# Performance work log

Measured on AMD Instinct MI355X. Metric: run time of the kernel, lower is better.

## Reference

```python
import jax, jax.numpy as jnp
import numpy as np

GROUPS = 32  # min(32, 256//4)
EPS = 1e-5


def setup_inputs() -> dict:
    key = jax.random.key(0)
    ks = jax.random.split(key, 4)
    B, C, H, W = 8, 256, 128, 128
    x = jax.random.normal(ks[0], (B, C, H, W), dtype=jnp.float32)
    gn_w = jnp.ones((C,), dtype=jnp.float32)
    gn_b = jnp.zeros((C,), dtype=jnp.float32)
    qkv_w = jax.random.normal(ks[1], (3 * C, C), dtype=jnp.float32) * (C ** -0.5)
    qkv_b = jnp.zeros((3 * C,), dtype=jnp.float32)
    proj_w = jax.random.normal(ks[2], (C, C), dtype=jnp.float32) * (C ** -0.5)
    proj_b = jnp.zeros((C,), dtype=jnp.float32)
    return {"x": x, "gn_w": gn_w, "gn_b": gn_b, "qkv_w": qkv_w,
            "qkv_b": qkv_b, "proj_w": proj_w, "proj_b": proj_b}


def _group_norm(x, w, b):
    B, C, H, W = x.shape
    xg = x.reshape(B, GROUPS, C // GROUPS, H, W)
    mean = xg.mean(axis=(2, 3, 4), keepdims=True)
    var = xg.var(axis=(2, 3, 4), keepdims=True)
    xg = (xg - mean) * jax.lax.rsqrt(var + EPS)
    x = xg.reshape(B, C, H, W)
    return x * w[None, :, None, None] + b[None, :, None, None]


def reference(x, gn_w, gn_b, qkv_w, qkv_b, proj_w, proj_b):
    B, C, H, W = x.shape
    num_heads = 8
    head_dim = C // num_heads
    scale = head_dim ** -0.5

    h = _group_norm(x, gn_w, gn_b)
    # 1x1 conv == per-pixel matmul over channels
    qkv = jnp.einsum('bchw,oc->bohw', h, qkv_w) + qkv_b[None, :, None, None]
    qkv = qkv.reshape(B, 3, num_heads, head_dim, H * W)
    q, k, v = qkv[:, 0], qkv[:, 1], qkv[:, 2]  # each (B, h, head_dim, HW)
    # Faithful to source: contracts over spatial axis d=HW -> (B,h,hd,hd)
    attn = jnp.einsum('bhid,bhjd->bhij', q, k) * scale
    attn = jax.nn.softmax(attn, axis=-1)
    out = jnp.einsum('bhij,bhjd->bhid', attn, v)  # (B, h, head_dim, HW)
    out = out.reshape(B, C, H, W)
    out = jnp.einsum('bchw,oc->bohw', out, proj_w) + proj_b[None, :, None, None]
    return x + out
```

## Files before the change

kernel.cpp:

```cpp
#include <hip/hip_runtime.h>
#include <stdint.h>

typedef __bf16 bf16;
typedef __attribute__((ext_vector_type(8))) __bf16 bf16x8;
typedef __attribute__((ext_vector_type(4))) float f32x4;

#define S_HW 16384
#define N_C 256

__device__ __forceinline__ f32x4 mfma16(bf16x8 a, bf16x8 b, f32x4 c) {
  return __builtin_amdgcn_mfma_f32_16x16x32_bf16(a, b, c, 0, 0, 0);
}
__device__ __forceinline__ void async_ld16(const bf16* g, bf16* l) {
  __builtin_amdgcn_global_load_lds(
      (const __attribute__((address_space(1))) unsigned int*)g,
      (__attribute__((address_space(3))) unsigned int*)l, 16, 0, 0);
}
__device__ __forceinline__ unsigned short bf2u(bf16 h) {
  union { bf16 h; unsigned short u; } c; c.h = h; return c.u;
}
__device__ __forceinline__ bf16 u2bf(unsigned short u) {
  union { unsigned short u; bf16 h; } c; c.u = u; return c.h;
}

__global__ __launch_bounds__(256) void k_split(
    const float* __restrict__ x, bf16* __restrict__ yhi, bf16* __restrict__ ylo,
    bf16* __restrict__ yt, float* __restrict__ Sx) {
  int b = blockIdx.z, c0 = blockIdx.y * 64, s0 = blockIdx.x * 64;
  __shared__ unsigned T[64][65];
  __shared__ float sxl[256];
  int t = threadIdx.x;
  int cl = t >> 2, sg = t & 3;
  size_t off = (size_t)(b * N_C + c0 + cl) * S_HW + s0 + sg * 16;
  const float* xp = x + off;
  bf16x8 hv[2], lv[2];
  float sum = 0.f;
#pragma unroll
  for (int i2 = 0; i2 < 4; i2++) {
    float4 v = *(const float4*)(xp + i2 * 4);
    float f4[4] = {v.x, v.y, v.z, v.w};
#pragma unroll
    for (int k = 0; k < 4; k++) {
      int i = i2 * 4 + k;
      float fv = f4[k];
      bf16 h = (bf16)fv;
      bf16 l = (bf16)(fv - (float)h);
      hv[i >> 3][i & 7] = h;
      lv[i >> 3][i & 7] = l;
      sum += fv;
      T[sg * 16 + i][cl] = (unsigned)bf2u(h) | ((unsigned)bf2u(l) << 16);
    }
  }
  *(bf16x8*)(yhi + off) = hv[0];
  *(bf16x8*)(yhi + off + 8) = hv[1];
  *(bf16x8*)(ylo + off) = lv[0];
  *(bf16x8*)(ylo + off + 8) = lv[1];
  sxl[t] = sum;
  __syncthreads();
  if (t < 64) {
    float s2 = sxl[t * 4] + sxl[t * 4 + 1] + sxl[t * 4 + 2] + sxl[t * 4 + 3];
    atomicAdd(&Sx[b * N_C + c0 + t], s2);
  }
  int sl = t >> 2, cg = t & 3;
  bf16x8 ho[2], lo2[2];
#pragma unroll
  for (int i = 0; i < 16; i++) {
    unsigned u = T[sl][cg * 16 + i];
    ho[i >> 3][i & 7] = u2bf((unsigned short)(u & 0xffffu));
    lo2[i >> 3][i & 7] = u2bf((unsigned short)(u >> 16));
  }
  size_t tb = (size_t)(b * S_HW + s0 + sl) * 512 + c0 + cg * 16;
  *(bf16x8*)(yt + tb) = ho[0];
  *(bf16x8*)(yt + tb + 8) = ho[1];
  *(bf16x8*)(yt + tb + 256) = lo2[0];
  *(bf16x8*)(yt + tb + 256 + 8) = lo2[1];
}

__global__ __launch_bounds__(256) void k_gram(
    const bf16* __restrict__ yhi, const bf16* __restrict__ ylo,
    float* __restrict__ YG3) {
  constexpr int BK = 32;
  constexpr int NT = 64;
  constexpr int BUF = 128 * BK;
  __shared__ __align__(16) bf16 As[3 * BUF];
  __shared__ __align__(16) bf16 Bs[3 * BUF];
  int kc = blockIdx.x * 2048;
  int m0 = (blockIdx.y >> 2) * 128, n0 = (blockIdx.y & 3) * 128;
  int b = blockIdx.z;
  int tid = threadIdx.x, lane = tid & 63, wave = tid >> 6;
  int wm = (wave >> 1) * 64, wn = (wave & 1) * 64;
  const bf16* Ab = yhi + (size_t)(b * N_C + m0) * S_HW;
  const bf16* Bb = (n0 < 256) ? yhi + (size_t)(b * N_C + n0) * S_HW
                              : ylo + (size_t)(b * N_C + n0 - 256) * S_HW;
  f32x4 acc[4][4] = {};
  int fm = lane & 15, fk = (lane >> 4) * 8;

  auto STAGE = [&](int bi, int t) {
    int kt = kc + t * BK;
#pragma unroll
    for (int i = 0; i < 2; i++) {
      int ch = i * 256 + tid;
      int row = ch >> 2, col = (ch & 3) * 8;
      async_ld16(Ab + (size_t)row * S_HW + kt + col,
                 As + bi * BUF + (i * 256 + wave * 64) * 8);
      async_ld16(Bb + (size_t)row * S_HW + kt + col,
                 Bs + bi * BUF + (i * 256 + wave * 64) * 8);
    }
  };

  STAGE(0, 0);
  STAGE(1, 1);
  STAGE(2, 2);
  int bi = 0;
  for (int t = 0; t < NT - 2; t++) {
    asm volatile("s_waitcnt vmcnt(8)" ::: "memory");
    __builtin_amdgcn_s_barrier();
    const bf16* Ap = As + bi * BUF;
    const bf16* Bp = Bs + bi * BUF;
    bf16x8 af[4], bfr[4];
#pragma unroll
    for (int q = 0; q < 4; q++) {
      af[q] = *(const bf16x8*)(Ap + (wm + q * 16 + fm) * BK + fk);
      bfr[q] = *(const bf16x8*)(Bp + (wn + q * 16 + fm) * BK + fk);
    }
    asm volatile("s_waitcnt lgkmcnt(0)" ::: "memory");
    __builtin_amdgcn_sched_barrier(0);
    __builtin_amdgcn_s_barrier();
    if (t + 3 < NT) STAGE(bi, t + 3);
#pragma unroll
    for (int ti = 0; ti < 4; ti++)
#pragma unroll
      for (int tj = 0; tj < 4; tj++)
        acc[ti][tj] = mfma16(af[ti], bfr[tj], acc[ti][tj]);
    bi = (bi == 2) ? 0 : bi + 1;
  }
#pragma unroll
  for (int pe = 0; pe < 2; pe++) {
    if (pe == 0)
      asm volatile("s_waitcnt vmcnt(4)" ::: "memory");
    else
      asm volatile("s_waitcnt vmcnt(0)" ::: "memory");
    __builtin_amdgcn_s_barrier();
    const bf16* Ap = As + bi * BUF;
    const bf16* Bp = Bs + bi * BUF;
    bf16x8 af[4], bfr[4];
#pragma unroll
    for (int q = 0; q < 4; q++) {
      af[q] = *(const bf16x8*)(Ap + (wm + q * 16 + fm) * BK + fk);
      bfr[q] = *(const bf16x8*)(Bp + (wn + q * 16 + fm) * BK + fk);
    }
#pragma unroll
    for (int ti = 0; ti < 4; ti++)
#pragma unroll
      for (int tj = 0; tj < 4; tj++)
        acc[ti][tj] = mfma16(af[ti], bfr[tj], acc[ti][tj]);
    bi = (bi == 2) ? 0 : bi + 1;
  }
  int quad = lane >> 4, cn = lane & 15;
#pragma unroll
  for (int ti = 0; ti < 4; ti++)
#pragma unroll
    for (int r = 0; r < 4; r++) {
      int m = m0 + wm + ti * 16 + quad * 4 + r;
#pragma unroll
      for (int tj = 0; tj < 4; tj++) {
        int n = n0 + wn + tj * 16 + cn;
        atomicAdd(&YG3[(size_t)(b * N_C + m) * 512 + n], acc[ti][tj][r]);
      }
    }
}

__global__ __launch_bounds__(256) void k_wkt(const float* __restrict__ qkv_w,
                                             float* __restrict__ WkT) {
  int k = blockIdx.x, j = threadIdx.x;
  WkT[k * 256 + j] = qkv_w[(256 + j) * 256 + k];
}

__global__ __launch_bounds__(256) void k_coefs(
    const float* __restrict__ Sx, const float* __restrict__ YG3,
    const float* __restrict__ gn_w, const float* __restrict__ gn_b,
    const float* __restrict__ qkv_w, const float* __restrict__ qkv_b,
    float* __restrict__ a_, float* __restrict__ bv_, float* __restrict__ u_,
    float* __restrict__ vbe) {
  int b = blockIdx.x, role = blockIdx.y, t = threadIdx.x;
  __shared__ float sxl[256], gxd[256], gm[32], gr[32], sh[256], bl[256];
  __shared__ float ured[64][4];
  sxl[t] = Sx[b * N_C + t];
  gxd[t] = YG3[(size_t)(b * N_C + t) * 512 + t] +
           2.f * YG3[(size_t)(b * N_C + t) * 512 + 256 + t];
  __syncthreads();
  if (t < 32) {
    float s = 0.f, q2 = 0.f;
#pragma unroll
    for (int i = 0; i < 8; i++) { s += sxl[t * 8 + i]; q2 += gxd[t * 8 + i]; }
    float mean = s * (1.f / 131072.f);
    float var = q2 * (1.f / 131072.f) - mean * mean;
    gm[t] = mean;
    gr[t] = 1.f / sqrtf(var + 1e-5f);
  }
  __syncthreads();
  {
    float A = gn_w[t] * gr[t >> 3];
    float B = gn_b[t] - gm[t >> 3] * A;
    bl[t] = B;
    sh[t] = A * sxl[t] + 16384.f * B;
    if (role == 0) {
      a_[b * N_C + t] = A;
      bv_[b * N_C + t] = B;
    }
  }
  __syncthreads();
  if (role == 0) {
    const float* wp = qkv_w + (size_t)(512 + t) * 256;
    float acc = 0.f;
    for (int c = 0; c < 256; c++) acc += wp[c] * bl[c];
    vbe[b * N_C + t] = acc + qkv_b[512 + t];
  } else {
    int r = (role - 1) * 64 + (t >> 2);
    int seg = (t & 3) * 64;
    const float* wp = qkv_w + (size_t)r * 256 + seg;
    float p = 0.f;
    for (int c = 0; c < 64; c++) p += wp[c] * sh[seg + c];
    ured[t >> 2][t & 3] = p;
    __syncthreads();
    if (t < 64)
      u_[b * 512 + (role - 1) * 64 + t] =
          ured[t][0] + ured[t][1] + ured[t][2] + ured[t][3];
  }
}

__global__ __launch_bounds__(256) void k_t1(
    const float* __restrict__ YG3, const float* __restrict__ WkT,
    const float* __restrict__ a_, const float* __restrict__ bv_,
    const float* __restrict__ Sx, float* __restrict__ T1) {
  int tile = blockIdx.x, b = blockIdx.y;
  int i0 = (tile >> 2) * 64, j0 = (tile & 3) * 64;
  __shared__ float As[64][69];
  __shared__ float Bs[64][69];
  __shared__ float al[256], bl[256], sxl[256];
  int t = threadIdx.x;
  al[t] = a_[b * N_C + t];
  bl[t] = bv_[b * N_C + t];
  sxl[t] = Sx[b * N_C + t];
  int cl = t >> 2, qq = (t & 3) * 16;
  int kk = t >> 2, jj = (t & 3) * 16;
  int ti = t >> 4, tj = t & 15;
  float acc[4][4] = {};
  for (int kc = 0; kc < 256; kc += 64) {
    {
      const float* yg = YG3 + (size_t)(b * N_C + i0 + cl) * 512 + kc + qq;
#pragma unroll
      for (int i = 0; i < 16; i++) As[cl][qq + i] = yg[i] + yg[256 + i];
    }
    __syncthreads();
    {
      int cp = kc + kk;
      const float* ygp = YG3 + (size_t)(b * N_C + cp) * 512 + 256 + i0 + jj;
#pragma unroll
      for (int i = 0; i < 16; i++) As[jj + i][kk] += ygp[i];
    }
    __syncthreads();
    {
      int c = i0 + cl;
      float ac = al[c], bc = bl[c], sxc = sxl[c];
#pragma unroll
      for (int i = 0; i < 16; i++) {
        int cp = kc + qq + i;
        As[cl][qq + i] = ac * al[cp] * As[cl][qq + i] + ac * bl[cp] * sxc +
                         bc * al[cp] * sxl[cp] + 16384.f * bc * bl[cp];
      }
    }
    {
      const float* wp = WkT + (size_t)(kc + kk) * 256 + j0 + jj;
#pragma unroll
      for (int i = 0; i < 16; i += 4) {
        float4 v = *(const float4*)(wp + i);
        Bs[kk][jj + i] = v.x; Bs[kk][jj + i + 1] = v.y;
        Bs[kk][jj + i + 2] = v.z; Bs[kk][jj + i + 3] = v.w;
      }
    }
    __syncthreads();
    for (int k = 0; k < 64; k++) {
      float av[4], bv4[4];
#pragma unroll
      for (int ii = 0; ii < 4; ii++) av[ii] = As[ti * 4 + ii][k];
#pragma unroll
      for (int j2 = 0; j2 < 4; j2++) bv4[j2] = Bs[k][tj * 4 + j2];
#pragma unroll
      for (int ii = 0; ii < 4; ii++)
#pragma unroll
        for (int j2 = 0; j2 < 4; j2++) acc[ii][j2] += av[ii] * bv4[j2];
    }
    __syncthreads();
  }
#pragma unroll
  for (int ii = 0; ii < 4; ii++)
#pragma unroll
    for (int j2 = 0; j2 < 4; j2++)
      T1[(size_t)(b * N_C + i0 + ti * 4 + ii) * 256 + j0 + tj * 4 + j2] =
          acc[ii][j2];
}

__global__ __launch_bounds__(256) void k_logits(
    const float* __restrict__ T1, const float* __restrict__ qkv_w,
    const float* __restrict__ qkv_b, const float* __restrict__ u_,
    float* __restrict__ attn) {
  int h = blockIdx.x, b = blockIdx.y;
  __shared__ float Tc[64][33];
  __shared__ float Wql[32][65];
  __shared__ float Ll[32][33];
  __shared__ float uq[32], uk[32], bq[32], bk[32];
  int t = threadIdx.x;
  if (t < 32) {
    uq[t] = u_[b * 512 + h * 32 + t];
    uk[t] = u_[b * 512 + 256 + h * 32 + t];
    bq[t] = qkv_b[h * 32 + t];
    bk[t] = qkv_b[256 + h * 32 + t];
  }
  int i = t & 31, jg = t >> 5;
  float acc[4] = {};
  for (int cc = 0; cc < 256; cc += 64) {
    {
      int c_l = t >> 2, seg = (t & 3) * 8;
      const float* tp = T1 + (size_t)(b * N_C + cc + c_l) * 256 + h * 32 + seg;
      float4 v0 = *(const float4*)tp, v1 = *(const float4*)(tp + 4);
      Tc[c_l][seg] = v0.x; Tc[c_l][seg + 1] = v0.y;
      Tc[c_l][seg + 2] = v0.z; Tc[c_l][seg + 3] = v0.w;
      Tc[c_l][seg + 4] = v1.x; Tc[c_l][seg + 5] = v1.y;
      Tc[c_l][seg + 6] = v1.z; Tc[c_l][seg + 7] = v1.w;
      int row = t >> 3, seg2 = (t & 7) * 8;
      const float* wp = qkv_w + (size_t)(h * 32 + row) * 256 + cc + seg2;
      float4 w0 = *(const float4*)wp, w1 = *(const float4*)(wp + 4);
      Wql[row][seg2] = w0.x; Wql[row][seg2 + 1] = w0.y;
      Wql[row][seg2 + 2] = w0.z; Wql[row][seg2 + 3] = w0.w;
      Wql[row][seg2 + 4] = w1.x; Wql[row][seg2 + 5] = w1.y;
      Wql[row][seg2 + 6] = w1.z; Wql[row][seg2 + 7] = w1.w;
    }
    __syncthreads();
    for (int c = 0; c < 64; c++) {
      float w = Wql[i][c];
#pragma unroll
      for (int j2 = 0; j2 < 4; j2++) acc[j2] += w * Tc[c][jg * 4 + j2];
    }
    __syncthreads();
  }
  const float scale = 0.17677669529663687f;
#pragma unroll
  for (int j2 = 0; j2 < 4; j2++) {
    int j = jg * 4 + j2;
    Ll[i][j] = scale * (acc[j2] + bq[i] * uk[j] + bk[j] * uq[i] +
                        16384.f * bq[i] * bk[j]);
  }
  __syncthreads();
  if (t < 32) {
    float m = -1e30f;
    for (int j = 0; j < 32; j++) m = fmaxf(m, Ll[t][j]);
    float e[32], s = 0.f;
    for (int j = 0; j < 32; j++) { e[j] = expf(Ll[t][j] - m); s += e[j]; }
    float inv = 1.f / s;
    float* ap = attn + (size_t)((b * 8 + h) * 32 + t) * 32;
    for (int j = 0; j < 32; j++) ap[j] = e[j] * inv;
  }
}

__global__ __launch_bounds__(256) void k_pv(
    const float* __restrict__ proj_w, const float* __restrict__ attn,
    const float* __restrict__ qkv_w, const float* __restrict__ a_,
    const float* __restrict__ vbe, const float* __restrict__ proj_b,
    bf16* __restrict__ FA, float* __restrict__ g_) {
  int tile = blockIdx.x, b = blockIdx.y;
  int i0 = (tile >> 2) * 64, j0 = (tile & 3) * 64;
  __shared__ float As[64][69];
  __shared__ float Bs[64][69];
  __shared__ float At[2][32][33];
  __shared__ float gred[64][4];
  int t = threadIdx.x;
  int cl = t >> 2, qq = (t & 3) * 16;
  int kk = t >> 2, jj = (t & 3) * 16;
  int ti = t >> 4, tj = t & 15;
  float acc[4][4] = {};
  float gacc = 0.f;
  for (int kc = 0; kc < 256; kc += 64) {
    int h0 = kc >> 5;
    __syncthreads();
    {
      const float* ap = attn + (size_t)b * 8192 + h0 * 1024;
#pragma unroll
      for (int i = 0; i < 8; i++) {
        int idx = t * 8 + i;
        At[idx >> 10][(idx >> 5) & 31][idx & 31] = ap[idx];
      }
      const float* wp = qkv_w + (size_t)(512 + kc + kk) * 256 + j0 + jj;
#pragma unroll
      for (int i = 0; i < 16; i += 4) {
        float4 v = *(const float4*)(wp + i);
        Bs[kk][jj + i] = v.x; Bs[kk][jj + i + 1] = v.y;
        Bs[kk][jj + i + 2] = v.z; Bs[kk][jj + i + 3] = v.w;
      }
    }
    __syncthreads();
    {
      int hl = qq >> 5;
      int jbase = qq & 31;
      const float* pp = proj_w + (size_t)(i0 + cl) * 256 + (h0 + hl) * 32;
      float pr[32];
#pragma unroll
      for (int i = 0; i < 32; i += 4) {
        float4 v = *(const float4*)(pp + i);
        pr[i] = v.x; pr[i + 1] = v.y; pr[i + 2] = v.z; pr[i + 3] = v.w;
      }
#pragma unroll
      for (int i = 0; i < 16; i++) {
        int jm = jbase + i;
        float s = 0.f;
#pragma unroll
        for (int ii = 0; ii < 32; ii++) s += pr[ii] * At[hl][ii][jm];
        As[cl][qq + i] = s;
        gacc += s * vbe[b * N_C + kc + qq + i];
      }
    }
    __syncthreads();
    for (int k = 0; k < 64; k++) {
      float av[4], bv4[4];
#pragma unroll
      for (int ii = 0; ii < 4; ii++) av[ii] = As[ti * 4 + ii][k];
#pragma unroll
      for (int j2 = 0; j2 < 4; j2++) bv4[j2] = Bs[k][tj * 4 + j2];
#pragma unroll
      for (int ii = 0; ii < 4; ii++)
#pragma unroll
        for (int j2 = 0; j2 < 4; j2++) acc[ii][j2] += av[ii] * bv4[j2];
    }
  }
  __syncthreads();
  gred[cl][t & 3] = gacc;
  __syncthreads();
  if ((tile & 3) == 0 && t < 64)
    g_[b * N_C + i0 + t] =
        gred[t][0] + gred[t][1] + gred[t][2] + gred[t][3] + proj_b[i0 + t];
  float a4[4];
  {
    float4 v = *(const float4*)(a_ + b * N_C + j0 + tj * 4);
    a4[0] = v.x; a4[1] = v.y; a4[2] = v.z; a4[3] = v.w;
  }
#pragma unroll
  for (int ii = 0; ii < 4; ii++) {
    int row = i0 + ti * 4 + ii;
#pragma unroll
    for (int j2 = 0; j2 < 4; j2++) {
      int col = j0 + tj * 4 + j2;
      float f = acc[ii][j2] * a4[j2] + (row == col ? 1.0f : 0.0f);
      bf16 hi = (bf16)f;
      bf16 lo = (bf16)(f - (float)hi);
      FA[(size_t)(b * N_C + row) * 512 + col] = hi;
      FA[(size_t)(b * N_C + row) * 512 + 256 + col] = lo;
    }
  }
}

__global__ __launch_bounds__(512) void k_final(
    const bf16* __restrict__ FA, const bf16* __restrict__ yt,
    const float* __restrict__ g_, float* __restrict__ out) {
  constexpr int BK = 64;
  constexpr int NT = 12;
  constexpr int BUFA = 256 * BK;
  constexpr int BUFB = 128 * BK;
  __shared__ __align__(16) bf16 As[3 * BUFA];
  __shared__ __align__(16) bf16 Bs[3 * BUFB];
  int b = blockIdx.z, n0 = blockIdx.x * 128;
  int tid = threadIdx.x, lane = tid & 63, wave = tid >> 6;
  int wm = (wave >> 1) * 64, wn = (wave & 1) * 64;
  const bf16* Ab = FA + (size_t)b * N_C * 512;
  const bf16* Bb = yt + (size_t)(b * S_HW + n0) * 512;
  f32x4 acc[4][4] = {};
  int fm = lane & 15, cs = lane >> 4;

  auto STAGE = [&](int bi, int t) {
    int kt = t * BK;
    int ka = (kt < 512) ? kt : kt - 512;
    int kb = (kt < 256) ? kt : kt - 256;
#pragma unroll
    for (int i = 0; i < 4; i++) {
      int ch = i * 512 + tid;
      int row = ch >> 3, slot = ch & 7;
      int gcol = (slot ^ (row & 7)) * 8;
      async_ld16(Ab + (size_t)row * 512 + ka + gcol,
                 As + bi * BUFA + ch * 8);
    }
#pragma unroll
    for (int i = 0; i < 2; i++) {
      int ch = i * 512 + tid;
      int row = ch >> 3, slot = ch & 7;
      int gcol = (slot ^ (row & 7)) * 8;
      async_ld16(Bb + (size_t)row * 512 + kb + gcol,
                 Bs + bi * BUFB + ch * 8);
    }
  };

  STAGE(0, 0);
  STAGE(1, 1);
  STAGE(2, 2);
  int bi = 0;
  for (int t = 0; t < NT - 2; t++) {
    asm volatile("s_waitcnt vmcnt(12)" ::: "memory");
    __builtin_amdgcn_s_barrier();
    const bf16* Ap = As + bi * BUFA;
    const bf16* Bp = Bs + bi * BUFB;
    bf16x8 af[4][2], bfr[4][2];
#pragma unroll
    for (int q = 0; q < 4; q++) {
      int ra = wm + q * 16 + fm;
      int rb = wn + q * 16 + fm;
#pragma unroll
      for (int h = 0; h < 2; h++) {
        af[q][h] = *(const bf16x8*)(Ap + ra * BK +
                                    (((h << 2) | cs) ^ (ra & 7)) * 8);
        bfr[q][h] = *(const bf16x8*)(Bp + rb * BK +
                                     (((h << 2) | cs) ^ (rb & 7)) * 8);
      }
    }
    asm volatile("s_waitcnt lgkmcnt(0)" ::: "memory");
    __builtin_amdgcn_sched_barrier(0);
    __builtin_amdgcn_s_barrier();
    if (t + 3 < NT) STAGE(bi, t + 3);
    __builtin_amdgcn_sched_barrier(0);
#pragma unroll
    for (int ti = 0; ti < 4; ti++)
#pragma unroll
      for (int tj = 0; tj < 4; tj++) {
        acc[ti][tj] = mfma16(af[ti][0], bfr[tj][0], acc[ti][tj]);
        acc[ti][tj] = mfma16(af[ti][1], bfr[tj][1], acc[ti][tj]);
      }
    bi = (bi == 2) ? 0 : bi + 1;
  }
#pragma unroll
  for (int pe = 0; pe < 2; pe++) {
    if (pe == 0)
      asm volatile("s_waitcnt vmcnt(6)" ::: "memory");
    else
      asm volatile("s_waitcnt vmcnt(0)" ::: "memory");
    __builtin_amdgcn_s_barrier();
    const bf16* Ap = As + bi * BUFA;
    const bf16* Bp = Bs + bi * BUFB;
    bf16x8 af[4][2], bfr[4][2];
#pragma unroll
    for (int q = 0; q < 4; q++) {
      int ra = wm + q * 16 + fm;
      int rb = wn + q * 16 + fm;
#pragma unroll
      for (int h = 0; h < 2; h++) {
        af[q][h] = *(const bf16x8*)(Ap + ra * BK +
                                    (((h << 2) | cs) ^ (ra & 7)) * 8);
        bfr[q][h] = *(const bf16x8*)(Bp + rb * BK +
                                     (((h << 2) | cs) ^ (rb & 7)) * 8);
      }
    }
#pragma unroll
    for (int ti = 0; ti < 4; ti++)
#pragma unroll
      for (int tj = 0; tj < 4; tj++) {
        acc[ti][tj] = mfma16(af[ti][0], bfr[tj][0], acc[ti][tj]);
        acc[ti][tj] = mfma16(af[ti][1], bfr[tj][1], acc[ti][tj]);
      }
    bi = (bi == 2) ? 0 : bi + 1;
  }
  int quad = lane >> 4, cn = lane & 15;
#pragma unroll
  for (int ti = 0; ti < 4; ti++)
#pragma unroll
    for (int r = 0; r < 4; r++) {
      int row = wm + ti * 16 + quad * 4 + r;
      float gb = g_[b * N_C + row];
#pragma unroll
      for (int tj = 0; tj < 4; tj++) {
        int col = n0 + wn + tj * 16 + cn;
        size_t idx = (size_t)(b * N_C + row) * S_HW + col;
        out[idx] = acc[ti][tj][r] + gb;
      }
    }
}

extern "C" void kernel_launch(void* const* d_in, const int* in_sizes, int n_in,
                              void* d_out, int out_size, void* d_ws,
                              size_t ws_size, hipStream_t stream) {
  const float* x = (const float*)d_in[0];
  const float* gn_w = (const float*)d_in[1];
  const float* gn_b = (const float*)d_in[2];
  const float* qkv_w = (const float*)d_in[3];
  const float* qkv_b = (const float*)d_in[4];
  const float* proj_w = (const float*)d_in[5];
  const float* proj_b = (const float*)d_in[6];
  float* out = (float*)d_out;

  const size_t MB = 1ull << 20;
  char* ws = (char*)d_ws;
  bf16* ylo = (bf16*)ws;
  bf16* yt = (bf16*)(ws + 64 * MB);
  float* YG3 = (float*)(ws + 192 * MB);
  bf16* FA = (bf16*)(ws + 194 * MB);
  float* WkT = (float*)(ws + 196 * MB);
  float* attn = (float*)(ws + 196 * MB + 256 * 1024);
  float* Sx = (float*)(ws + 196 * MB + 512 * 1024);
  float* a_ = (float*)(ws + 196 * MB + 520 * 1024);
  float* bv_ = (float*)(ws + 196 * MB + 528 * 1024);
  float* u_ = (float*)(ws + 196 * MB + 536 * 1024);
  float* vbe = (float*)(ws + 196 * MB + 552 * 1024);
  float* g_ = (float*)(ws + 196 * MB + 560 * 1024);
  float* T1 = (float*)(ws + 198 * MB);
  bf16* yhi = (bf16*)d_out;

  if (ws_size < 200 * MB) return;

  hipMemsetAsync(YG3, 0, 4 * MB + 520 * 1024, stream);
  k_split<<<dim3(256, 4, 8), 256, 0, stream>>>(x, yhi, ylo, yt, Sx);
  k_gram<<<dim3(8, 8, 8), 256, 0, stream>>>(yhi, ylo, YG3);
  k_wkt<<<256, 256, 0, stream>>>(qkv_w, WkT);
  k_coefs<<<dim3(8, 9), 256, 0, stream>>>(Sx, YG3, gn_w, gn_b, qkv_w, qkv_b,
                                          a_, bv_, u_, vbe);
  k_t1<<<dim3(16, 8), 256, 0, stream>>>(YG3, WkT, a_, bv_, Sx, T1);
  k_logits<<<dim3(8, 8), 256, 0, stream>>>(T1, qkv_w, qkv_b, u_, attn);
  k_pv<<<dim3(16, 8), 256, 0, stream>>>(proj_w, attn, qkv_w, a_, vbe, proj_b,
                                        FA, g_);
  k_final<<<dim3(128, 1, 8), 512, 0, stream>>>(FA, yt, g_, out);
}
```

Measured before the change: 520.9 us.

## Enlarge Gram kernel tile to 256x256 with XOR-swizzled LDS and double buffering

Result: no change. 516.1 us (-0.9%).

```diff
diff --git a/kernel.cpp b/kernel.cpp
--- a/kernel.cpp
+++ b/kernel.cpp
@@ -76,96 +76,89 @@
   *(bf16x8*)(yt + tb + 256 + 8) = lo2[1];
 }
 
-__global__ __launch_bounds__(256) void k_gram(
+__global__ __launch_bounds__(512, 2) void k_gram(
     const bf16* __restrict__ yhi, const bf16* __restrict__ ylo,
     float* __restrict__ YG3) {
-  constexpr int BK = 32;
-  constexpr int NT = 64;
-  constexpr int BUF = 128 * BK;
-  __shared__ __align__(16) bf16 As[3 * BUF];
-  __shared__ __align__(16) bf16 Bs[3 * BUF];
-  int kc = blockIdx.x * 2048;
-  int m0 = (blockIdx.y >> 2) * 128, n0 = (blockIdx.y & 3) * 128;
+  constexpr int BK = 64;
+  constexpr int NT = 16;
+  constexpr int BUF = 256 * BK;
+  __shared__ __align__(16) bf16 As[2 * BUF];
+  __shared__ __align__(16) bf16 Bs[2 * BUF];
+  int kc = blockIdx.x * 1024;
+  int nsel = blockIdx.y;
   int b = blockIdx.z;
   int tid = threadIdx.x, lane = tid & 63, wave = tid >> 6;
-  int wm = (wave >> 1) * 64, wn = (wave & 1) * 64;
-  const bf16* Ab = yhi + (size_t)(b * N_C + m0) * S_HW;
-  const bf16* Bb = (n0 < 256) ? yhi + (size_t)(b * N_C + n0) * S_HW
-                              : ylo + (size_t)(b * N_C + n0 - 256) * S_HW;
-  f32x4 acc[4][4] = {};
-  int fm = lane & 15, fk = (lane >> 4) * 8;
+  int wm = (wave >> 1) * 64, wn = (wave & 1) * 128;
+  const bf16* Ab = yhi + (size_t)(b * N_C) * S_HW;
+  const bf16* Bb = (nsel == 0 ? yhi : ylo) + (size_t)(b * N_C) * S_HW;
+  f32x4 acc[4][8] = {};
+  int fm = lane & 15, cs = lane >> 4;
 
   auto STAGE = [&](int bi, int t) {
     int kt = kc + t * BK;
 #pragma unroll
-    for (int i = 0; i < 2; i++) {
-      int ch = i * 256 + tid;
-      int row = ch >> 2, col = (ch & 3) * 8;
-      async_ld16(Ab + (size_t)row * S_HW + kt + col,
-                 As + bi * BUF + (i * 256 + wave * 64) * 8);
-      async_ld16(Bb + (size_t)row * S_HW + kt + col,
-                 Bs + bi * BUF + (i * 256 + wave * 64) * 8);
+    for (int i = 0; i < 4; i++) {
+      int ch = i * 512 + tid;
+      int row = ch >> 3, slot = ch & 7;
+      int gcol = (slot ^ (row & 7)) * 8;
+      async_ld16(Ab + (size_t)row * S_HW + kt + gcol, As + bi * BUF + ch * 8);
+      async_ld16(Bb + (size_t)row * S_HW + kt + gcol, Bs + bi * BUF + ch * 8);
     }
   };
 
   STAGE(0, 0);
   STAGE(1, 1);
-  STAGE(2, 2);
-  int bi = 0;
-  for (int t = 0; t < NT - 2; t++) {
-    asm volatile("s_waitcnt vmcnt(8)" ::: "memory");
+  int cur = 0;
+  for (int t = 0; t < NT; t++) {
+    if (t < NT - 1)
+      asm volatile("s_waitcnt vmcnt(8)" ::: "memory");
+    else
+      asm volatile("s_waitcnt vmcnt(0)" ::: "memory");
     __builtin_amdgcn_s_barrier();
-    const bf16* Ap = As + bi * BUF;
-    const bf16* Bp = Bs + bi * BUF;
-    bf16x8 af[4], bfr[4];
+    const bf16* Ap = As + cur * BUF;
+    const bf16* Bp = Bs + cur * BUF;
+    bf16x8 af[4][2], bfr[8][2];
 #pragma unroll
     for (int q = 0; q < 4; q++) {
-      af[q] = *(const bf16x8*)(Ap + (wm + q * 16 + fm) * BK + fk);
-      bfr[q] = *(const bf16x8*)(Bp + (wn + q * 16 + fm) * BK + fk);
+      int ra = wm + q * 16 + fm;
+#pragma unroll
+      for (int h = 0; h < 2; h++)
+        af[q][h] =
+            *(const bf16x8*)(Ap + ra * BK + (((h << 2) | cs) ^ (ra & 7)) * 8);
+    }
+#pragma unroll
+    for (int p = 0; p < 8; p++) {
+      int rb = wn + p * 16 + fm;
+#pragma unroll
+      for (int h = 0; h < 2; h++)
+        bfr[p][h] =
+            *(const bf16x8*)(Bp + rb * BK + (((h << 2) | cs) ^ (rb & 7)) * 8);
     }
     asm volatile("s_waitcnt lgkmcnt(0)" ::: "memory");
     __builtin_amdgcn_sched_barrier(0);
     __builtin_amdgcn_s_barrier();
-    if (t + 3 < NT) STAGE(bi, t + 3);
-#pragma unroll
-    for (int ti = 0; ti < 4; ti++)
-#pragma unroll
-      for (int tj = 0; tj < 4; tj++)
-        acc[ti][tj] = mfma16(af[ti], bfr[tj], acc[ti][tj]);
-    bi = (bi == 2) ? 0 : bi + 1;
-  }
-#pragma unroll
-  for (int pe = 0; pe < 2; pe++) {
-    if (pe == 0)
-      asm volatile("s_waitcnt vmcnt(4)" ::: "memory");
-    else
-      asm volatile("s_waitcnt vmcnt(0)" ::: "memory");
-    __builtin_amdgcn_s_barrier();
-    const bf16* Ap = As + bi * BUF;
-    const bf16* Bp = Bs + bi * BUF;
-    bf16x8 af[4], bfr[4];
-#pragma unroll
-    for (int q = 0; q < 4; q++) {
-      af[q] = *(const bf16x8*)(Ap + (wm + q * 16 + fm) * BK + fk);
-      bfr[q] = *(const bf16x8*)(Bp + (wn + q * 16 + fm) * BK + fk);
-    }
-#pragma unroll
-    for (int ti = 0; ti < 4; ti++)
-#pragma unroll
-      for (int tj = 0; tj < 4; tj++)
-        acc[ti][tj] = mfma16(af[ti], bfr[tj], acc[ti][tj]);
-    bi = (bi == 2) ? 0 : bi + 1;
+    if (t + 2 < NT) STAGE(cur, t + 2);
+    __builtin_amdgcn_sched_barrier(0);
+#pragma unroll
+    for (int q = 0; q < 4; q++)
+#pragma unroll
+      for (int p = 0; p < 8; p++) {
+        acc[q][p] = mfma16(af[q][0], bfr[p][0], acc[q][p]);
+        acc[q][p] = mfma16(af[q][1], bfr[p][1], acc[q][p]);
+      }
+    cur ^= 1;
   }
   int quad = lane >> 4, cn = lane & 15;
-#pragma unroll
-  for (int ti = 0; ti < 4; ti++)
+  float* yg = YG3 + (size_t)(b * N_C) * 512 + nsel * 256;
+#pragma unroll
+  for (int q = 0; q < 4; q++)
 #pragma unroll
     for (int r = 0; r < 4; r++) {
-      int m = m0 + wm + ti * 16 + quad * 4 + r;
-#pragma unroll
-      for (int tj = 0; tj < 4; tj++) {
-        int n = n0 + wn + tj * 16 + cn;
-        atomicAdd(&YG3[(size_t)(b * N_C + m) * 512 + n], acc[ti][tj][r]);
+      int m = wm + q * 16 + quad * 4 + r;
+#pragma unroll
+      for (int p = 0; p < 8; p++) {
+        int n = wn + p * 16 + cn;
+        atomicAdd(&yg[(size_t)m * 512 + n], acc[q][p][r]);
       }
     }
 }
@@ -613,7 +606,7 @@
 
   hipMemsetAsync(YG3, 0, 4 * MB + 520 * 1024, stream);
   k_split<<<dim3(256, 4, 8), 256, 0, stream>>>(x, yhi, ylo, yt, Sx);
-  k_gram<<<dim3(8, 8, 8), 256, 0, stream>>>(yhi, ylo, YG3);
+  k_gram<<<dim3(16, 2, 8), 512, 0, stream>>>(yhi, ylo, YG3);
   k_wkt<<<256, 256, 0, stream>>>(qkv_w, WkT);
   k_coefs<<<dim3(8, 9), 256, 0, stream>>>(Sx, YG3, gn_w, gn_b, qkv_w, qkv_b,
                                           a_, bv_, u_, vbe);
```
